# Performance work log

Hardware: AMD Instinct MI355X
Metric: run time of the kernel (lower is better)

The kernel has to match this reference:

```python
import jax, jax.numpy as jnp
import numpy as np

N_Q = 8          # number of residual quantizer stages
N_CODES = 1024   # 2 ** (75 // N_q + 1)
D = 128
GAMMA = 0.99


def setup_inputs() -> dict:
    key = jax.random.key(0)
    k1, k2, k3, k4 = jax.random.split(key, 4)
    data_object = jax.random.normal(k1, (16, D, 2048), dtype=jnp.float32)
    weights = jax.random.normal(k2, (N_Q, N_CODES, D), dtype=jnp.float32)
    # EMA cluster-size buffer; scale so most codes are 'alive' (>= 2)
    N_i = jax.random.uniform(k3, (N_Q, N_CODES), dtype=jnp.float32) * 100.0
    m_i = jax.random.normal(k4, (N_Q, N_CODES, D), dtype=jnp.float32)
    return {"data_object": data_object, "weights": weights, "N_i": N_i, "m_i": m_i}


def reference(data_object, weights, N_i, m_i):
    b, d, s = data_object.shape
    y = jnp.transpose(data_object, (0, 2, 1))  # [b, s, D]
    residual = y
    cur_y = jnp.zeros_like(y)
    all_idx, new_Ni, new_mi, new_W = [], [], [], []
    key = jax.random.key(42)
    one_m_g = 1.0 - GAMMA
    for i in range(N_Q):
        W = weights[i]  # [N, D]
        # squared euclidean distances: ||y||^2 + ||W||^2 - 2 y.W^T  -> [b, s, N]
        dist = ((residual ** 2).sum(-1)[..., None]
                + (W ** 2).sum(-1)[None, None, :]
                - 2.0 * jnp.einsum('bsd,nd->bsn', residual, W))
        idx = jnp.argmin(dist, axis=-1)          # [b, s]
        Q = W[idx]                               # gather  [b, s, D]
        cur_y = cur_y + Q
        flat_idx = idx.reshape(-1)               # [b*s]
        flat_res = residual.reshape(-1, d)       # [b*s, D]
        # fused scatter-reduce replacing the torch per-code mask loop
        counts = jax.ops.segment_sum(jnp.ones(flat_idx.shape, jnp.float32),
                                     flat_idx, num_segments=N_CODES)
        sums = jax.ops.segment_sum(flat_res, flat_idx, num_segments=N_CODES)
        Ni_new = N_i[i] * GAMMA + counts * one_m_g
        mi_new = m_i[i] * GAMMA + sums * one_m_g
        w_new = mi_new / jnp.clip(Ni_new, 1e-8)[:, None]
        # dead-code replacement with random residual vectors
        dead = Ni_new < 2.0
        rid = jax.random.randint(jax.random.fold_in(key, i), (N_CODES,),
                                 0, flat_res.shape[0])
        w_new = jnp.where(dead[:, None], flat_res[rid], w_new)
        all_idx.append(idx)
        new_Ni.append(Ni_new)
        new_mi.append(mi_new)
        new_W.append(w_new)
        residual = residual - Q
    cur_y_t = jnp.transpose(cur_y, (0, 2, 1))  # [b, D, s]
    # straight-through estimator
    logits = data_object + jax.lax.stop_gradient(cur_y_t - data_object)
    commitment_loss = jnp.mean((jax.lax.stop_gradient(cur_y_t) - data_object) ** 2)
    indices = jnp.stack(all_idx, axis=0)  # [N_q, b, s]
    return (logits, commitment_loss, indices,
            jnp.stack(new_Ni), jnp.stack(new_mi), jnp.stack(new_W))
```

## Files before the change

kernel.cpp:

```cpp
#include <hip/hip_runtime.h>
#include <hip/hip_bf16.h>

#define NQ 8
#define NC 1024
#define DD 128
#define BB 16
#define SS 2048
#define RR (BB * SS)
#define GAMMA_F 0.99f
#define TAU 0.03f

typedef __attribute__((ext_vector_type(8))) short bf16x8;
typedef __attribute__((ext_vector_type(4))) float f32x4;

__device__ __forceinline__ ushort f2bf(float x) {
  __hip_bfloat16 b = __float2bfloat16(x);
  return *reinterpret_cast<ushort*>(&b);
}
__device__ __forceinline__ float bf2f(ushort u) {
  unsigned v = ((unsigned)u) << 16;
  return *reinterpret_cast<float*>(&v);
}

__global__ __launch_bounds__(256) void k_transpose_in(
    const float* __restrict__ data, float* __restrict__ res)
{
  __shared__ float tile[32][33];
  int b = blockIdx.z;
  int s0 = blockIdx.x << 5, d0 = blockIdx.y << 5;
  int tx = threadIdx.x, ty = threadIdx.y;
  #pragma unroll
  for (int r = 0; r < 32; r += 8)
    tile[ty + r][tx] = data[((size_t)b * DD + d0 + ty + r) * SS + s0 + tx];
  __syncthreads();
  #pragma unroll
  for (int r = 0; r < 32; r += 8)
    res[((size_t)b * SS + s0 + ty + r) * DD + d0 + tx] = tile[tx][ty + r];
}

__global__ void k_wsq(const float* __restrict__ W, float* __restrict__ wsq)
{
  int c = blockIdx.x * blockDim.x + threadIdx.x;
  if (c >= NQ * NC) return;
  const float4* p = reinterpret_cast<const float4*>(W + (size_t)c * DD);
  float s = 0.f;
  #pragma unroll 8
  for (int k = 0; k < DD / 4; ++k) {
    float4 v = p[k];
    s += v.x * v.x + v.y * v.y + v.z * v.z + v.w * v.w;
  }
  wsq[c] = s;
}

__global__ __launch_bounds__(256) void k_split(
    const float* __restrict__ src, ushort* __restrict__ dst)
{
  int i = blockIdx.x * 256 + threadIdx.x;
  int row = i >> 2, ks = i & 3;
  const float4* sp = reinterpret_cast<const float4*>(src + (size_t)row * DD + ks * 32);
  size_t gb = ((size_t)(row >> 4) * 8 + ks * 2) * 64 + (row & 15);
  #pragma unroll
  for (int kg = 0; kg < 4; ++kg) {
    float4 a = sp[kg * 2], b = sp[kg * 2 + 1];
    ushort4 h0, h1, l0, l1;
    h0.x = f2bf(a.x); l0.x = f2bf(a.x - bf2f(h0.x));
    h0.y = f2bf(a.y); l0.y = f2bf(a.y - bf2f(h0.y));
    h0.z = f2bf(a.z); l0.z = f2bf(a.z - bf2f(h0.z));
    h0.w = f2bf(a.w); l0.w = f2bf(a.w - bf2f(h0.w));
    h1.x = f2bf(b.x); l1.x = f2bf(b.x - bf2f(h1.x));
    h1.y = f2bf(b.y); l1.y = f2bf(b.y - bf2f(h1.y));
    h1.z = f2bf(b.z); l1.z = f2bf(b.z - bf2f(h1.z));
    h1.w = f2bf(b.w); l1.w = f2bf(b.w - bf2f(h1.w));
    ushort* ph = dst + (gb + kg * 16) * 8;
    *reinterpret_cast<ushort4*>(ph) = h0;
    *reinterpret_cast<ushort4*>(ph + 4) = h1;
    ushort* pl = ph + 64 * 8;
    *reinterpret_cast<ushort4*>(pl) = l0;
    *reinterpret_cast<ushort4*>(pl + 4) = l1;
  }
}

__global__ __launch_bounds__(256, 2) void k_argmin(
    float* __restrict__ res, ushort* __restrict__ res_hl,
    const ushort* __restrict__ w_hl, const float* __restrict__ W,
    const float* __restrict__ wsq,
    int* __restrict__ idxw, float* __restrict__ idxf,
    int* __restrict__ count, int* __restrict__ fb_count,
    int* __restrict__ fb_list, int stage)
{
  __shared__ float Lm1[4][16], Lm2[4][16];
  __shared__ int   Li1[4][16];
  __shared__ int   sidx[16];

  const int t = threadIdx.x;
  const int l = t & 63;
  const int w = t >> 6;
  const int l15 = l & 15, kg = l >> 4;
  const int row0 = blockIdx.x * 16;
  const float* wsqs = wsq + stage * NC;
  const ushort* wb = w_hl + (size_t)stage * NC * 256;

  const size_t ab = (size_t)blockIdx.x * 8;
  bf16x8 ah[4], al[4];
  #pragma unroll
  for (int ks = 0; ks < 4; ++ks) {
    ah[ks] = *reinterpret_cast<const bf16x8*>(res_hl + ((ab + ks * 2) * 64 + l) * 8);
    al[ks] = *reinterpret_cast<const bf16x8*>(res_hl + ((ab + ks * 2 + 1) * 64 + l) * 8);
  }

  float m1[4], m2[4];
  int i1[4];
  #pragma unroll
  for (int rg = 0; rg < 4; ++rg) { m1[rg] = 3.4e38f; m2[rg] = 3.4e38f; i1[rg] = 0; }

  #pragma unroll 1
  for (int k8 = 0; k8 < 8; ++k8) {
    const int ct0 = w * 16 + k8 * 2;
    const size_t b0 = (size_t)ct0 * 8;
    const size_t b1 = b0 + 8;
    bf16x8 bh0[4], bl0[4], bh1[4], bl1[4];
    #pragma unroll
    for (int ks = 0; ks < 4; ++ks) {
      bh0[ks] = *reinterpret_cast<const bf16x8*>(wb + ((b0 + ks * 2) * 64 + l) * 8);
      bl0[ks] = *reinterpret_cast<const bf16x8*>(wb + ((b0 + ks * 2 + 1) * 64 + l) * 8);
      bh1[ks] = *reinterpret_cast<const bf16x8*>(wb + ((b1 + ks * 2) * 64 + l) * 8);
      bl1[ks] = *reinterpret_cast<const bf16x8*>(wb + ((b1 + ks * 2 + 1) * 64 + l) * 8);
    }
    f32x4 p0 = {0.f, 0.f, 0.f, 0.f};
    f32x4 q0 = {0.f, 0.f, 0.f, 0.f};
    f32x4 p1 = {0.f, 0.f, 0.f, 0.f};
    f32x4 q1 = {0.f, 0.f, 0.f, 0.f};
    #pragma unroll
    for (int ks = 0; ks < 4; ++ks) {
      p0 = __builtin_amdgcn_mfma_f32_16x16x32_bf16(ah[ks], bh0[ks], p0, 0, 0, 0);
      p1 = __builtin_amdgcn_mfma_f32_16x16x32_bf16(ah[ks], bh1[ks], p1, 0, 0, 0);
      q0 = __builtin_amdgcn_mfma_f32_16x16x32_bf16(al[ks], bh0[ks], q0, 0, 0, 0);
      q1 = __builtin_amdgcn_mfma_f32_16x16x32_bf16(al[ks], bh1[ks], q1, 0, 0, 0);
      q0 = __builtin_amdgcn_mfma_f32_16x16x32_bf16(ah[ks], bl0[ks], q0, 0, 0, 0);
      q1 = __builtin_amdgcn_mfma_f32_16x16x32_bf16(ah[ks], bl1[ks], q1, 0, 0, 0);
    }
    int code0 = ct0 * 16 + l15;
    float sq0 = wsqs[code0];
    float sq1 = wsqs[code0 + 16];
    #pragma unroll
    for (int rg = 0; rg < 4; ++rg) {
      float s0 = fmaf(-2.f, p0[rg] + q0[rg], sq0);
      if (s0 < m1[rg]) { m2[rg] = m1[rg]; m1[rg] = s0; i1[rg] = code0; }
      else if (s0 < m2[rg]) m2[rg] = s0;
      float s1 = fmaf(-2.f, p1[rg] + q1[rg], sq1);
      if (s1 < m1[rg]) { m2[rg] = m1[rg]; m1[rg] = s1; i1[rg] = code0 + 16; }
      else if (s1 < m2[rg]) m2[rg] = s1;
    }
  }

  #pragma unroll
  for (int mk = 1; mk <= 8; mk <<= 1) {
    #pragma unroll
    for (int rg = 0; rg < 4; ++rg) {
      float om1 = __shfl_xor(m1[rg], mk);
      int   oi  = __shfl_xor(i1[rg], mk);
      float om2 = __shfl_xor(m2[rg], mk);
      bool bwin = (om1 < m1[rg]) || (om1 == m1[rg] && oi < i1[rg]);
      float lose = bwin ? m1[rg] : om1;
      m2[rg] = fminf(fminf(m2[rg], om2), lose);
      if (bwin) { m1[rg] = om1; i1[rg] = oi; }
    }
  }
  if (l15 == 0) {
    #pragma unroll
    for (int rg = 0; rg < 4; ++rg) {
      Lm1[w][kg * 4 + rg] = m1[rg];
      Lm2[w][kg * 4 + rg] = m2[rg];
      Li1[w][kg * 4 + rg] = i1[rg];
    }
  }
  __syncthreads();

  if (t < 16) {
    float gm1 = Lm1[0][t], gm2 = Lm2[0][t];
    int gi = Li1[0][t];
    #pragma unroll
    for (int q = 1; q < 4; ++q) {
      float b1 = Lm1[q][t], b2 = Lm2[q][t];
      int bi = Li1[q][t];
      bool bwin = (b1 < gm1) || (b1 == gm1 && bi < gi);
      float lose = bwin ? gm1 : b1;
      gm2 = fminf(fminf(gm2, b2), lose);
      if (bwin) { gm1 = b1; gi = bi; }
    }
    int row = row0 + t;
    idxw[row] = gi;
    idxf[row] = (float)gi;
    sidx[t] = gi;
    if (gm2 - gm1 > TAU) {
      atomicAdd(&count[gi], 1);
    } else {
      int p = atomicAdd(fb_count, 1);
      fb_list[p] = row;
    }
  }
  __syncthreads();

  {
    int rloc = t >> 4, g = t & 15;
    int row = row0 + rloc;
    int id = sidx[rloc];
    const float4* rp = reinterpret_cast<const float4*>(res + (size_t)row * DD + g * 8);
    const float4* qp = reinterpret_cast<const float4*>(W + ((size_t)stage * NC + id) * DD + g * 8);
    float4 r0 = rp[0], r1 = rp[1];
    float4 q0 = qp[0], q1 = qp[1];
    float4 o0, o1;
    o0.x = r0.x - q0.x; o0.y = r0.y - q0.y; o0.z = r0.z - q0.z; o0.w = r0.w - q0.w;
    o1.x = r1.x - q1.x; o1.y = r1.y - q1.y; o1.z = r1.z - q1.z; o1.w = r1.w - q1.w;
    float4* wp2 = reinterpret_cast<float4*>(res + (size_t)row * DD + g * 8);
    wp2[0] = o0; wp2[1] = o1;
    ushort4 h0, h1, l0, l1;
    h0.x = f2bf(o0.x); l0.x = f2bf(o0.x - bf2f(h0.x));
    h0.y = f2bf(o0.y); l0.y = f2bf(o0.y - bf2f(h0.y));
    h0.z = f2bf(o0.z); l0.z = f2bf(o0.z - bf2f(h0.z));
    h0.w = f2bf(o0.w); l0.w = f2bf(o0.w - bf2f(h0.w));
    h1.x = f2bf(o1.x); l1.x = f2bf(o1.x - bf2f(h1.x));
    h1.y = f2bf(o1.y); l1.y = f2bf(o1.y - bf2f(h1.y));
    h1.z = f2bf(o1.z); l1.z = f2bf(o1.z - bf2f(h1.z));
    h1.w = f2bf(o1.w); l1.w = f2bf(o1.w - bf2f(h1.w));
    int ks = g >> 2, kgg = g & 3;
    size_t gb = ((size_t)(row >> 4) * 8 + ks * 2) * 64 + kgg * 16 + (row & 15);
    ushort* ph = res_hl + gb * 8;
    *reinterpret_cast<ushort4*>(ph) = h0;
    *reinterpret_cast<ushort4*>(ph + 4) = h1;
    ushort* pl = ph + 64 * 8;
    *reinterpret_cast<ushort4*>(pl) = l0;
    *reinterpret_cast<ushort4*>(pl + 4) = l1;
  }
}

__global__ __launch_bounds__(256) void k_fallback(
    float* __restrict__ res, ushort* __restrict__ res_hl,
    const float* __restrict__ W, const float* __restrict__ wsq,
    const int* __restrict__ fb_count, const int* __restrict__ fb_list,
    int* __restrict__ idxw, float* __restrict__ idxf,
    int* __restrict__ count, int stage)
{
  __shared__ float rr[128];
  __shared__ float sv[256];
  __shared__ int   si[256];
  int n = *fb_count;
  int t = threadIdx.x;
  for (int b = blockIdx.x; b < n; b += gridDim.x) {
    int row = fb_list[b];
    int approx = idxw[row];
    __syncthreads();
    if (t < 128)
      rr[t] = res[(size_t)row * DD + t] + W[((size_t)stage * NC + approx) * DD + t];
    __syncthreads();
    float bm = 3.4e38f; int bi = 0;
    #pragma unroll
    for (int j = 0; j < 4; ++j) {
      int c = t + j * 256;
      const float4* wp = reinterpret_cast<const float4*>(W + ((size_t)stage * NC + c) * DD);
      float dot = 0.f;
      #pragma unroll 8
      for (int k = 0; k < 32; ++k) {
        float4 wv = wp[k];
        dot = fmaf(rr[4 * k + 0], wv.x, dot);
        dot = fmaf(rr[4 * k + 1], wv.y, dot);
        dot = fmaf(rr[4 * k + 2], wv.z, dot);
        dot = fmaf(rr[4 * k + 3], wv.w, dot);
      }
      float s = fmaf(-2.f, dot, wsq[stage * NC + c]);
      if (s < bm || (s == bm && c < bi)) { bm = s; bi = c; }
    }
    sv[t] = bm; si[t] = bi;
    __syncthreads();
    for (int sft = 128; sft > 0; sft >>= 1) {
      if (t < sft) {
        float ov = sv[t + sft]; int oi = si[t + sft];
        if (ov < sv[t] || (ov == sv[t] && oi < si[t])) { sv[t] = ov; si[t] = oi; }
      }
      __syncthreads();
    }
    int win = si[0];
    if (t == 0) {
      idxw[row] = win;
      idxf[row] = (float)win;
      atomicAdd(&count[win], 1);
    }
    if (t < 128) {
      float o = rr[t] - W[((size_t)stage * NC + win) * DD + t];
      res[(size_t)row * DD + t] = o;
      ushort hi = f2bf(o);
      ushort lo = f2bf(o - bf2f(hi));
      size_t g0 = ((size_t)(row >> 4) * 8 + (t >> 5) * 2) * 64 + ((t >> 3) & 3) * 16 + (row & 15);
      res_hl[g0 * 8 + (t & 7)] = hi;
      res_hl[(g0 + 64) * 8 + (t & 7)] = lo;
    }
  }
}

__global__ __launch_bounds__(1024) void k_scan(
    int* __restrict__ count, int* __restrict__ offs, int* __restrict__ pos)
{
  __shared__ int sc[1024];
  int t = threadIdx.x;
  sc[t] = count[t];
  __syncthreads();
  for (int off = 1; off < 1024; off <<= 1) {
    int v = (t >= off) ? sc[t - off] : 0;
    __syncthreads();
    sc[t] += v;
    __syncthreads();
  }
  offs[t + 1] = sc[t];
  if (t == 0) { offs[0] = 0; count[1024] = 0; }
  pos[t] = 0;
  count[t] = 0;
}

__global__ __launch_bounds__(256) void k_scatter(
    const int* __restrict__ idxw, const int* __restrict__ offs,
    int* __restrict__ pos, int* __restrict__ rows_sorted)
{
  int r = blockIdx.x * 256 + threadIdx.x;
  int c = idxw[r];
  int slot = offs[c] + atomicAdd(&pos[c], 1);
  rows_sorted[slot] = r;
}

__device__ __forceinline__ unsigned rotl32(unsigned v, int r) { return (v << r) | (v >> (32 - r)); }

__device__ void threefry2x32(unsigned ks0, unsigned ks1, unsigned x0, unsigned x1,
                             unsigned& o0, unsigned& o1)
{
  unsigned ks2 = ks0 ^ ks1 ^ 0x1BD11BDAu;
  x0 += ks0; x1 += ks1;
  x0 += x1; x1 = rotl32(x1, 13); x1 ^= x0;
  x0 += x1; x1 = rotl32(x1, 15); x1 ^= x0;
  x0 += x1; x1 = rotl32(x1, 26); x1 ^= x0;
  x0 += x1; x1 = rotl32(x1, 6);  x1 ^= x0;
  x0 += ks1; x1 += ks2 + 1u;
  x0 += x1; x1 = rotl32(x1, 17); x1 ^= x0;
  x0 += x1; x1 = rotl32(x1, 29); x1 ^= x0;
  x0 += x1; x1 = rotl32(x1, 16); x1 ^= x0;
  x0 += x1; x1 = rotl32(x1, 24); x1 ^= x0;
  x0 += ks2; x1 += ks0 + 2u;
  x0 += x1; x1 = rotl32(x1, 13); x1 ^= x0;
  x0 += x1; x1 = rotl32(x1, 15); x1 ^= x0;
  x0 += x1; x1 = rotl32(x1, 26); x1 ^= x0;
  x0 += x1; x1 = rotl32(x1, 6);  x1 ^= x0;
  x0 += ks0; x1 += ks1 + 3u;
  x0 += x1; x1 = rotl32(x1, 17); x1 ^= x0;
  x0 += x1; x1 = rotl32(x1, 29); x1 ^= x0;
  x0 += x1; x1 = rotl32(x1, 16); x1 ^= x0;
  x0 += x1; x1 = rotl32(x1, 24); x1 ^= x0;
  x0 += ks1; x1 += ks2 + 4u;
  x0 += x1; x1 = rotl32(x1, 13); x1 ^= x0;
  x0 += x1; x1 = rotl32(x1, 15); x1 ^= x0;
  x0 += x1; x1 = rotl32(x1, 26); x1 ^= x0;
  x0 += x1; x1 = rotl32(x1, 6);  x1 ^= x0;
  x0 += ks2; x1 += ks0 + 5u;
  o0 = x0; o1 = x1;
}

__global__ __launch_bounds__(1024) void k_finalize(
    const float* __restrict__ Ni_in, const float* __restrict__ mi_in,
    const int* __restrict__ offs, const int* __restrict__ rows_sorted,
    const float* __restrict__ res, const float* __restrict__ W,
    const int* __restrict__ idxw,
    float* __restrict__ outNi, float* __restrict__ outmi, float* __restrict__ outW,
    int stage)
{
  __shared__ float red[8][128];
  const float ONEMG = (float)(1.0 - 0.99);
  int c = blockIdx.x;
  int t = threadIdx.x;
  int d = t & 127;
  int jw = t >> 7;
  int base = offs[c];
  int cnt = offs[c + 1] - base;
  const int* rs = rows_sorted + base;

  float sum = 0.f;
  int j = jw;
  for (; j + 24 < cnt; j += 32) {
    int r0 = rs[j];
    int r1 = rs[j + 8];
    int r2 = rs[j + 16];
    int r3 = rs[j + 24];
    float v0 = res[(size_t)r0 * DD + d];
    float v1 = res[(size_t)r1 * DD + d];
    float v2 = res[(size_t)r2 * DD + d];
    float v3 = res[(size_t)r3 * DD + d];
    sum += v0 + v1 + v2 + v3;
  }
  for (; j < cnt; j += 8)
    sum += res[(size_t)rs[j] * DD + d];

  red[jw][d] = sum;
  __syncthreads();

  if (jw == 0) {
    float s8 = red[0][d] + red[1][d] + red[2][d] + red[3][d]
             + red[4][d] + red[5][d] + red[6][d] + red[7][d];
    float wc = W[((size_t)stage * NC + c) * DD + d];
    float sum_pre = fmaf((float)cnt, wc, s8);
    float ni = Ni_in[stage * NC + c] * GAMMA_F + (float)cnt * ONEMG;
    float mm = mi_in[((size_t)stage * NC + c) * DD + d] * GAMMA_F + sum_pre * ONEMG;
    float w = mm / fmaxf(ni, 1e-8f);
    if (ni < 2.0f) {
      unsigned K0, K1, a0, a1, b0, b1, o0, o1;
      threefry2x32(0u, 42u, 0u, (unsigned)stage, K0, K1);
      threefry2x32(K0, K1, 0u, 2u, a0, a1);
      threefry2x32(K0, K1, 1u, 3u, b0, b1);
      unsigned bits;
      if (c < 512) { threefry2x32(a1, b1, (unsigned)c, (unsigned)(c + 512), o0, o1); bits = o0; }
      else         { threefry2x32(a1, b1, (unsigned)(c - 512), (unsigned)c, o0, o1); bits = o1; }
      int rid = (int)(bits & 32767u);
      int idr = idxw[rid];
      w = res[(size_t)rid * DD + d] + W[((size_t)stage * NC + idr) * DD + d];
    }
    if (d == 0) outNi[stage * NC + c] = ni;
    size_t o = ((size_t)stage * NC + c) * DD + d;
    outmi[o] = mm;
    outW[o] = w;
  }
}

__global__ __launch_bounds__(256) void k_final(
    const float* __restrict__ data, const float* __restrict__ res,
    float* __restrict__ logits, float* __restrict__ partials)
{
  __shared__ float tile[32][33];
  __shared__ float wsum[4];
  int b = blockIdx.z, s0 = blockIdx.x << 5, d0 = blockIdx.y << 5;
  int tx = threadIdx.x, ty = threadIdx.y;
  #pragma unroll
  for (int r = 0; r < 32; r += 8)
    tile[ty + r][tx] = res[((size_t)b * SS + s0 + ty + r) * DD + d0 + tx];
  __syncthreads();
  float l = 0.f;
  #pragma unroll
  for (int r = 0; r < 32; r += 8) {
    int dv = d0 + ty + r, s = s0 + tx;
    size_t o = ((size_t)b * DD + dv) * SS + s;
    float rv = tile[tx][ty + r];
    logits[o] = data[o] - rv;
    l = fmaf(rv, rv, l);
  }
  #pragma unroll
  for (int m = 1; m < 64; m <<= 1) l += __shfl_xor(l, m);
  int lin = ty * 32 + tx;
  if ((lin & 63) == 0) wsum[lin >> 6] = l;
  __syncthreads();
  if (lin == 0) {
    int bl = (blockIdx.z * gridDim.y + blockIdx.y) * gridDim.x + blockIdx.x;
    partials[bl] = wsum[0] + wsum[1] + wsum[2] + wsum[3];
  }
}

__global__ __launch_bounds__(1024) void k_loss_reduce(
    const float* __restrict__ partials, float* __restrict__ loss)
{
  __shared__ float ws[16];
  int t = threadIdx.x;
  float s = partials[t] + partials[t + 1024] + partials[t + 2048] + partials[t + 3072];
  #pragma unroll
  for (int m = 1; m < 64; m <<= 1) s += __shfl_xor(s, m);
  if ((t & 63) == 0) ws[t >> 6] = s;
  __syncthreads();
  if (t < 16) {
    float v = ws[t];
    #pragma unroll
    for (int m = 1; m < 16; m <<= 1) v += __shfl_xor(v, m);
    if (t == 0) loss[0] = v * (1.0f / 4194304.0f);
  }
}

extern "C" void kernel_launch(void* const* d_in, const int* in_sizes, int n_in,
                              void* d_out, int out_size, void* d_ws, size_t ws_size,
                              hipStream_t stream)
{
  (void)in_sizes; (void)n_in; (void)out_size; (void)ws_size;
  const float* data = (const float*)d_in[0];
  const float* W    = (const float*)d_in[1];
  const float* Ni   = (const float*)d_in[2];
  const float* mi   = (const float*)d_in[3];

  float* out        = (float*)d_out;
  float* out_logits = out;
  float* out_loss   = out + (size_t)BB * DD * SS;
  float* out_idx    = out_loss + 1;
  float* out_Ni     = out_idx + (size_t)NQ * RR;
  float* out_mi     = out_Ni + (size_t)NQ * NC;
  float* out_W      = out_mi + (size_t)NQ * NC * DD;

  char* wp = (char*)d_ws;
  float*  resA        = (float*)wp;   wp += (size_t)RR * DD * 4;
  ushort* res_hl      = (ushort*)wp;  wp += (size_t)RR * DD * 4;
  ushort* w_hl        = (ushort*)wp;  wp += (size_t)NQ * NC * DD * 4;
  float*  wsq         = (float*)wp;   wp += (size_t)NQ * NC * 4;
  int*    idxw        = (int*)wp;     wp += (size_t)RR * 4;
  int*    fb_list     = (int*)wp;     wp += (size_t)RR * 4;
  int*    rows_sorted = (int*)wp;     wp += (size_t)RR * 4;
  int*    count       = (int*)wp;     wp += (size_t)1025 * 4;
  int*    fb_count    = count + 1024;
  int*    pos         = (int*)wp;     wp += (size_t)NC * 4;
  int*    offs        = (int*)wp;     wp += (size_t)(NC + 1) * 4;
  float*  partials    = (float*)wp;   wp += (size_t)4096 * 4;

  k_transpose_in<<<dim3(SS / 32, DD / 32, BB), dim3(32, 8), 0, stream>>>(data, resA);
  k_split<<<RR * 4 / 256, 256, 0, stream>>>(resA, res_hl);
  k_wsq<<<(NQ * NC + 255) / 256, 256, 0, stream>>>(W, wsq);
  k_split<<<NQ * NC * 4 / 256, 256, 0, stream>>>(W, w_hl);
  hipMemsetAsync(count, 0, 1025 * sizeof(int), stream);

  for (int i = 0; i < NQ; ++i) {
    k_argmin<<<RR / 16, 256, 0, stream>>>(resA, res_hl, w_hl, W, wsq, idxw,
                                          out_idx + (size_t)i * RR,
                                          count, fb_count, fb_list, i);
    k_fallback<<<512, 256, 0, stream>>>(resA, res_hl, W, wsq, fb_count, fb_list,
                                        idxw, out_idx + (size_t)i * RR, count, i);
    k_scan<<<1, 1024, 0, stream>>>(count, offs, pos);
    k_scatter<<<RR / 256, 256, 0, stream>>>(idxw, offs, pos, rows_sorted);
    k_finalize<<<NC, 1024, 0, stream>>>(Ni, mi, offs, rows_sorted, resA, W, idxw,
                                        out_Ni, out_mi, out_W, i);
  }

  k_final<<<dim3(SS / 32, DD / 32, BB), dim3(32, 8), 0, stream>>>(data, resA, out_logits, partials);
  k_loss_reduce<<<1, 1024, 0, stream>>>(partials, out_loss);
}
```

Before: 876.3 us.

## Keep codebook slices register-resident and split argmin into partial plus merge kernels

The argmin kernel now holds each wave's fixed 32-code slice of the codebook in registers and loops over row tiles, so each block reads the weights once and streams residual tiles past them. Each slice writes a per-row partial best, second-best and index to global buffers, and a new merge kernel reduces the 32 partials per row and then does the existing count, fallback and residual update. This removes the repeated codebook reloads per row tile. In exchange it adds a large global round trip of partials (32×RR entries in each of three arrays) and one extra kernel launch per stage.

New measurement: 1.037 ms. 1.18x slower.

```diff
diff --git a/kernel.cpp b/kernel.cpp
--- a/kernel.cpp
+++ b/kernel.cpp
@@ -80,45 +80,24 @@
   }
 }
 
-__global__ __launch_bounds__(256, 2) void k_argmin(
-    float* __restrict__ res, ushort* __restrict__ res_hl,
-    const ushort* __restrict__ w_hl, const float* __restrict__ W,
+__global__ __launch_bounds__(512, 1) void k_argmin(
+    const ushort* __restrict__ res_hl, const ushort* __restrict__ w_hl,
     const float* __restrict__ wsq,
-    int* __restrict__ idxw, float* __restrict__ idxf,
-    int* __restrict__ count, int* __restrict__ fb_count,
-    int* __restrict__ fb_list, int stage)
-{
-  __shared__ float Lm1[4][16], Lm2[4][16];
-  __shared__ int   Li1[4][16];
-  __shared__ int   sidx[16];
-
+    float* __restrict__ pm1, float* __restrict__ pm2, int* __restrict__ pi1,
+    int stage)
+{
   const int t = threadIdx.x;
   const int l = t & 63;
   const int w = t >> 6;
   const int l15 = l & 15, kg = l >> 4;
-  const int row0 = blockIdx.x * 16;
+  const int sl32 = blockIdx.y * 8 + w;
+  const int ct0g = sl32 * 2;
   const float* wsqs = wsq + stage * NC;
   const ushort* wb = w_hl + (size_t)stage * NC * 256;
 
-  const size_t ab = (size_t)blockIdx.x * 8;
-  bf16x8 ah[4], al[4];
-  #pragma unroll
-  for (int ks = 0; ks < 4; ++ks) {
-    ah[ks] = *reinterpret_cast<const bf16x8*>(res_hl + ((ab + ks * 2) * 64 + l) * 8);
-    al[ks] = *reinterpret_cast<const bf16x8*>(res_hl + ((ab + ks * 2 + 1) * 64 + l) * 8);
-  }
-
-  float m1[4], m2[4];
-  int i1[4];
-  #pragma unroll
-  for (int rg = 0; rg < 4; ++rg) { m1[rg] = 3.4e38f; m2[rg] = 3.4e38f; i1[rg] = 0; }
-
-  #pragma unroll 1
-  for (int k8 = 0; k8 < 8; ++k8) {
-    const int ct0 = w * 16 + k8 * 2;
-    const size_t b0 = (size_t)ct0 * 8;
-    const size_t b1 = b0 + 8;
-    bf16x8 bh0[4], bl0[4], bh1[4], bl1[4];
+  bf16x8 bh0[4], bl0[4], bh1[4], bl1[4];
+  {
+    size_t b0 = (size_t)ct0g * 8, b1 = b0 + 8;
     #pragma unroll
     for (int ks = 0; ks < 4; ++ks) {
       bh0[ks] = *reinterpret_cast<const bf16x8*>(wb + ((b0 + ks * 2) * 64 + l) * 8);
@@ -126,6 +105,27 @@
       bh1[ks] = *reinterpret_cast<const bf16x8*>(wb + ((b1 + ks * 2) * 64 + l) * 8);
       bl1[ks] = *reinterpret_cast<const bf16x8*>(wb + ((b1 + ks * 2 + 1) * 64 + l) * 8);
     }
+  }
+  int code0 = ct0g * 16 + l15;
+  float sq0 = wsqs[code0];
+  float sq1 = wsqs[code0 + 16];
+
+  #pragma unroll 1
+  for (int rt = blockIdx.x; rt < RR / 16; rt += 256) {
+    asm volatile("" : "+v"(bh0[0]), "+v"(bh0[1]), "+v"(bh0[2]), "+v"(bh0[3]),
+                      "+v"(bl0[0]), "+v"(bl0[1]), "+v"(bl0[2]), "+v"(bl0[3]));
+    asm volatile("" : "+v"(bh1[0]), "+v"(bh1[1]), "+v"(bh1[2]), "+v"(bh1[3]),
+                      "+v"(bl1[0]), "+v"(bl1[1]), "+v"(bl1[2]), "+v"(bl1[3]));
+    asm volatile("" : "+v"(sq0), "+v"(sq1));
+
+    const size_t ab = (size_t)rt * 8;
+    bf16x8 ah[4], al[4];
+    #pragma unroll
+    for (int ks = 0; ks < 4; ++ks) {
+      ah[ks] = *reinterpret_cast<const bf16x8*>(res_hl + ((ab + ks * 2) * 64 + l) * 8);
+      al[ks] = *reinterpret_cast<const bf16x8*>(res_hl + ((ab + ks * 2 + 1) * 64 + l) * 8);
+    }
+
     f32x4 p0 = {0.f, 0.f, 0.f, 0.f};
     f32x4 q0 = {0.f, 0.f, 0.f, 0.f};
     f32x4 p1 = {0.f, 0.f, 0.f, 0.f};
@@ -139,56 +139,72 @@
       q0 = __builtin_amdgcn_mfma_f32_16x16x32_bf16(ah[ks], bl0[ks], q0, 0, 0, 0);
       q1 = __builtin_amdgcn_mfma_f32_16x16x32_bf16(ah[ks], bl1[ks], q1, 0, 0, 0);
     }
-    int code0 = ct0 * 16 + l15;
-    float sq0 = wsqs[code0];
-    float sq1 = wsqs[code0 + 16];
+
+    float m1[4], m2[4];
+    int i1[4];
     #pragma unroll
     for (int rg = 0; rg < 4; ++rg) {
       float s0 = fmaf(-2.f, p0[rg] + q0[rg], sq0);
-      if (s0 < m1[rg]) { m2[rg] = m1[rg]; m1[rg] = s0; i1[rg] = code0; }
-      else if (s0 < m2[rg]) m2[rg] = s0;
       float s1 = fmaf(-2.f, p1[rg] + q1[rg], sq1);
-      if (s1 < m1[rg]) { m2[rg] = m1[rg]; m1[rg] = s1; i1[rg] = code0 + 16; }
-      else if (s1 < m2[rg]) m2[rg] = s1;
-    }
-  }
-
-  #pragma unroll
-  for (int mk = 1; mk <= 8; mk <<= 1) {
-    #pragma unroll
-    for (int rg = 0; rg < 4; ++rg) {
-      float om1 = __shfl_xor(m1[rg], mk);
-      int   oi  = __shfl_xor(i1[rg], mk);
-      float om2 = __shfl_xor(m2[rg], mk);
-      bool bwin = (om1 < m1[rg]) || (om1 == m1[rg] && oi < i1[rg]);
-      float lose = bwin ? m1[rg] : om1;
-      m2[rg] = fminf(fminf(m2[rg], om2), lose);
-      if (bwin) { m1[rg] = om1; i1[rg] = oi; }
-    }
-  }
-  if (l15 == 0) {
-    #pragma unroll
-    for (int rg = 0; rg < 4; ++rg) {
-      Lm1[w][kg * 4 + rg] = m1[rg];
-      Lm2[w][kg * 4 + rg] = m2[rg];
-      Li1[w][kg * 4 + rg] = i1[rg];
-    }
-  }
-  __syncthreads();
+      bool w0 = (s0 <= s1);
+      m1[rg] = w0 ? s0 : s1;
+      m2[rg] = w0 ? s1 : s0;
+      i1[rg] = w0 ? code0 : (code0 + 16);
+    }
+
+    #pragma unroll
+    for (int mk = 1; mk <= 8; mk <<= 1) {
+      #pragma unroll
+      for (int rg = 0; rg < 4; ++rg) {
+        float om1 = __shfl_xor(m1[rg], mk);
+        int   oi  = __shfl_xor(i1[rg], mk);
+        float om2 = __shfl_xor(m2[rg], mk);
+        bool bwin = (om1 < m1[rg]) || (om1 == m1[rg] && oi < i1[rg]);
+        float lose = bwin ? m1[rg] : om1;
+        m2[rg] = fminf(fminf(m2[rg], om2), lose);
+        if (bwin) { m1[rg] = om1; i1[rg] = oi; }
+      }
+    }
+    if (l15 == 0) {
+      #pragma unroll
+      for (int rg = 0; rg < 4; ++rg) {
+        int row = rt * 16 + kg * 4 + rg;
+        size_t o = (size_t)sl32 * RR + row;
+        pm1[o] = m1[rg];
+        pm2[o] = m2[rg];
+        pi1[o] = i1[rg];
+      }
+    }
+  }
+}
+
+__global__ __launch_bounds__(256) void k_merge_update(
+    float* __restrict__ res, ushort* __restrict__ res_hl,
+    const float* __restrict__ W,
+    const float* __restrict__ pm1, const float* __restrict__ pm2,
+    const int* __restrict__ pi1,
+    int* __restrict__ idxw, float* __restrict__ idxf,
+    int* __restrict__ count, int* __restrict__ fb_count,
+    int* __restrict__ fb_list, int stage)
+{
+  __shared__ int sidx[16];
+  const int t = threadIdx.x;
+  const int row0 = blockIdx.x * 16;
 
   if (t < 16) {
-    float gm1 = Lm1[0][t], gm2 = Lm2[0][t];
-    int gi = Li1[0][t];
-    #pragma unroll
-    for (int q = 1; q < 4; ++q) {
-      float b1 = Lm1[q][t], b2 = Lm2[q][t];
-      int bi = Li1[q][t];
+    int row = row0 + t;
+    float gm1 = pm1[row], gm2 = pm2[row];
+    int gi = pi1[row];
+    #pragma unroll 4
+    for (int s = 1; s < 32; ++s) {
+      size_t o = (size_t)s * RR + row;
+      float b1 = pm1[o], b2 = pm2[o];
+      int bi = pi1[o];
       bool bwin = (b1 < gm1) || (b1 == gm1 && bi < gi);
       float lose = bwin ? gm1 : b1;
       gm2 = fminf(fminf(gm2, b2), lose);
       if (bwin) { gm1 = b1; gi = bi; }
     }
-    int row = row0 + t;
     idxw[row] = gi;
     idxf[row] = (float)gi;
     sidx[t] = gi;
@@ -498,6 +514,9 @@
   ushort* res_hl      = (ushort*)wp;  wp += (size_t)RR * DD * 4;
   ushort* w_hl        = (ushort*)wp;  wp += (size_t)NQ * NC * DD * 4;
   float*  wsq         = (float*)wp;   wp += (size_t)NQ * NC * 4;
+  float*  pm1         = (float*)wp;   wp += (size_t)32 * RR * 4;
+  float*  pm2         = (float*)wp;   wp += (size_t)32 * RR * 4;
+  int*    pi1         = (int*)wp;     wp += (size_t)32 * RR * 4;
   int*    idxw        = (int*)wp;     wp += (size_t)RR * 4;
   int*    fb_list     = (int*)wp;     wp += (size_t)RR * 4;
   int*    rows_sorted = (int*)wp;     wp += (size_t)RR * 4;
@@ -514,9 +533,10 @@
   hipMemsetAsync(count, 0, 1025 * sizeof(int), stream);
 
   for (int i = 0; i < NQ; ++i) {
-    k_argmin<<<RR / 16, 256, 0, stream>>>(resA, res_hl, w_hl, W, wsq, idxw,
-                                          out_idx + (size_t)i * RR,
-                                          count, fb_count, fb_list, i);
+    k_argmin<<<dim3(256, 4), 512, 0, stream>>>(res_hl, w_hl, wsq, pm1, pm2, pi1, i);
+    k_merge_update<<<RR / 16, 256, 0, stream>>>(resA, res_hl, W, pm1, pm2, pi1,
+                                                idxw, out_idx + (size_t)i * RR,
+                                                count, fb_count, fb_list, i);
     k_fallback<<<512, 256, 0, stream>>>(resA, res_hl, W, wsq, fb_count, fb_list,
                                         idxw, out_idx + (size_t)i * RR, count, i);
     k_scan<<<1, 1024, 0, stream>>>(count, offs, pos);
```
